# Performance work log

Measured on AMD Instinct MI355X. Metric: run time of the kernel, lower is better.

## Reference

```python
import jax, jax.numpy as jnp
import numpy as np

N_NODES = 50000
N_EDGES = 800000
N_ATOMS = 100
HID = 128
N_LAYERS = 3
OUT_LAYERS = 2
OUT_DIM = 1
N_GRAPHS = 1024
EPS = 1e-12  # F.normalize eps


def setup_inputs() -> dict:
    key = jax.random.key(0)
    ks = jax.random.split(key, 12)
    s = 0.05
    x_ori = jax.random.randint(ks[0], (N_NODES,), 0, N_ATOMS)
    edge_index = jax.random.randint(ks[1], (2, N_EDGES), 0, N_NODES)
    edge_attr = jax.random.normal(ks[2], (N_EDGES, 1), jnp.float32)
    batch_ids = jnp.sort(jax.random.randint(ks[3], (N_NODES,), 0, N_GRAPHS))
    embd_w = jax.random.normal(ks[4], (N_ATOMS, HID), jnp.float32) * s
    gamma_w = jnp.ones((N_LAYERS, N_ATOMS, 1), jnp.float32)  # reset_parameters sets ones
    w_atom_W = jax.random.normal(ks[5], (N_LAYERS, HID, HID), jnp.float32) * s
    w_atom_b = jax.random.normal(ks[6], (N_LAYERS, HID), jnp.float32) * s
    lin_W = jax.random.normal(ks[7], (OUT_LAYERS, HID, HID), jnp.float32) * s
    lin_b = jax.random.normal(ks[8], (OUT_LAYERS, HID), jnp.float32) * s
    wp_W = jax.random.normal(ks[9], (HID, OUT_DIM), jnp.float32) * s
    wp_b = jax.random.normal(ks[10], (OUT_DIM,), jnp.float32) * s
    return dict(x_ori=x_ori, edge_index=edge_index, edge_attr=edge_attr,
                batch_ids=batch_ids, embd_w=embd_w, gamma_w=gamma_w,
                w_atom_W=w_atom_W, w_atom_b=w_atom_b, lin_W=lin_W, lin_b=lin_b,
                wp_W=wp_W, wp_b=wp_b)


def reference(x_ori, edge_index, edge_attr, batch_ids, embd_w, gamma_w,
              w_atom_W, w_atom_b, lin_W, lin_b, wp_W, wp_b):
    src, dst = edge_index[0], edge_index[1]
    x = embd_w[x_ori]  # [N, H]
    for l in range(N_LAYERS):
        h = jax.nn.relu(x @ w_atom_W[l] + w_atom_b[l])            # [N, H]
        gam = jax.nn.sigmoid(gamma_w[l])[x_ori][dst]              # [E, 1]
        ew = jnp.exp(-gam * edge_attr ** 2)                       # [E, 1]
        msg = ew * h[src]                                         # [E, H] gather+weight
        agg = jax.ops.segment_sum(msg, dst, num_segments=N_NODES) # scatter-add
        y = agg + x
        nrm = jnp.maximum(jnp.linalg.norm(y, axis=1, keepdims=True), EPS)
        x = y / nrm                                               # F.normalize(., 2, 1)
    for i in range(OUT_LAYERS):
        x = jax.nn.relu(x @ lin_W[i] + lin_b[i])
    m_x = jax.ops.segment_sum(x, batch_ids, num_segments=N_GRAPHS)  # [G, H]
    props = m_x @ wp_W + wp_b                                      # [G, 1]
    return jnp.squeeze(props, axis=1)                              # [G]
```

## Files before the change

### kernel.cpp

```cpp
#include <hip/hip_runtime.h>
#include <hip/hip_bf16.h>
#include <math.h>

typedef __hip_bfloat16 bf16;
typedef unsigned int uint;
typedef unsigned short ushort;
typedef __attribute__((ext_vector_type(8))) short short8;
typedef __attribute__((ext_vector_type(4))) float f32x4;

#define HID 128
#define NN 50000
#define NE 800000
#define NG 1024
#define NA 100
#define CAP 64

#define NB   98
#define RCAP 10240

__device__ __forceinline__ uint bf16_rne_hi(float f) {
    uint u = __float_as_uint(f);
    return (u + 0x7fffu + ((u >> 16) & 1u)) & 0xffff0000u;
}
__device__ __forceinline__ uint pack_bf16x2(float lo, float hi) {
    return (bf16_rne_hi(lo) >> 16) | bf16_rne_hi(hi);
}
__device__ __forceinline__ ushort bf16_rne(float f) {
    uint u = __float_as_uint(f);
    return (ushort)((u + 0x7fffu + ((u >> 16) & 1u)) >> 16);
}
__device__ __forceinline__ float lof(uint u) { return __uint_as_float(u << 16); }
__device__ __forceinline__ float hif(uint u) { return __uint_as_float(u & 0xffff0000u); }
__device__ __forceinline__ float load_f(const void* p, int i, int f32) {
    return f32 ? ((const float*)p)[i]
               : __uint_as_float((uint)((const ushort*)p)[i] << 16);
}
__device__ __forceinline__ int detect_f32(const void* emb) {
    const ushort* p = (const ushort*)emb;
    int lane = threadIdx.x & 63;
    float v = __uint_as_float((uint)p[lane * 4] << 16);
    int bad0 = (!(v == v) || fabsf(v) > 1e4f || (v != 0.0f && fabsf(v) < 1e-10f));
    float w = __uint_as_float((uint)p[lane * 4 + 2] << 16);
    int bad1 = (!(w == w) || fabsf(w) > 1e4f || (w != 0.0f && fabsf(w) < 1e-10f));
    int cnt = __popcll(__ballot(bad0)) + __popcll(__ballot(bad1));
    return cnt > 16;
}

#define A_BLKS     196
#define EMB_BLKS   ((NN * 64) / 256)
#define PACKW_BLKS (5 * 16384 / 256)
#define CVT_CNT    (300 + 384 + 256 + 128 + 1)
#define CVT_BLKS   5
#define PR_B1      A_BLKS
#define PR_B2      (PR_B1 + EMB_BLKS)
#define PR_B3      (PR_B2 + PACKW_BLKS)
#define PR_B4      (PR_B3 + CVT_BLKS)
#define PR_B5      (PR_B4 + 4)
#define PREP_GRID  (PR_B5 + 1)

__global__ void prep_k(const int* __restrict__ xo, const void* __restrict__ emb,
                       const void* __restrict__ gamw, const void* __restrict__ wAW,
                       const void* __restrict__ wAb, const void* __restrict__ linW,
                       const void* __restrict__ linb, const void* __restrict__ wpW,
                       const void* __restrict__ wpb,
                       const int* __restrict__ esrc, const int* __restrict__ edst,
                       const void* __restrict__ ea,
                       uint* __restrict__ xb, ushort* __restrict__ Wp,
                       float* __restrict__ f_sgam, float* __restrict__ f_wAb,
                       float* __restrict__ f_linb, float* __restrict__ f_wp,
                       float* __restrict__ f_wpb,
                       uint2* __restrict__ rec, int* __restrict__ bcur,
                       float* __restrict__ gpn,
                       float* __restrict__ grf, int* __restrict__ flag) {
    int f32 = detect_f32(emb);
    int b = blockIdx.x, t = threadIdx.x;
    if (b < PR_B1) {
        __shared__ int hist[NB];
        __shared__ int obase[NB];
        if (t < NB) hist[t] = 0;
        __syncthreads();
        int  dv[16];
        uint rv[16];
#pragma unroll
        for (int k = 0; k < 4; ++k) {
            int e = b * 4096 + k * 1024 + t * 4;
            if (e + 3 < NE) {
                int4 s4 = *(const int4*)(esrc + e);
                int4 d4 = *(const int4*)(edst + e);
                float a0, a1, a2, a3;
                if (f32) {
                    float4 f = *(const float4*)((const float*)ea + e);
                    a0 = f.x; a1 = f.y; a2 = f.z; a3 = f.w;
                } else {
                    ushort4 u = *(const ushort4*)((const ushort*)ea + e);
                    a0 = __uint_as_float((uint)u.x << 16);
                    a1 = __uint_as_float((uint)u.y << 16);
                    a2 = __uint_as_float((uint)u.z << 16);
                    a3 = __uint_as_float((uint)u.w << 16);
                }
                atomicAdd(&hist[d4.x >> 9], 1);
                atomicAdd(&hist[d4.y >> 9], 1);
                atomicAdd(&hist[d4.z >> 9], 1);
                atomicAdd(&hist[d4.w >> 9], 1);
                dv[k * 4 + 0] = d4.x; rv[k * 4 + 0] = (uint)(s4.x & 0xffff) | ((uint)bf16_rne(a0 * a0) << 16);
                dv[k * 4 + 1] = d4.y; rv[k * 4 + 1] = (uint)(s4.y & 0xffff) | ((uint)bf16_rne(a1 * a1) << 16);
                dv[k * 4 + 2] = d4.z; rv[k * 4 + 2] = (uint)(s4.z & 0xffff) | ((uint)bf16_rne(a2 * a2) << 16);
                dv[k * 4 + 3] = d4.w; rv[k * 4 + 3] = (uint)(s4.w & 0xffff) | ((uint)bf16_rne(a3 * a3) << 16);
            } else {
                dv[k * 4 + 0] = dv[k * 4 + 1] = dv[k * 4 + 2] = dv[k * 4 + 3] = -1;
                rv[k * 4 + 0] = rv[k * 4 + 1] = rv[k * 4 + 2] = rv[k * 4 + 3] = 0;
            }
        }
        __syncthreads();
        if (t < NB) {
            int c = hist[t];
            obase[t] = c ? atomicAdd(&bcur[t], c) : 0;
            hist[t] = 0;
        }
        __syncthreads();
#pragma unroll
        for (int k = 0; k < 16; ++k) {
            int d = dv[k];
            if (d >= 0) {
                int bb = d >> 9;
                int r = atomicAdd(&hist[bb], 1);
                int idx = obase[bb] + r;
                if (idx < RCAP) rec[bb * RCAP + idx] = make_uint2(rv[k], (uint)d);
            }
        }
    } else if (b < PR_B2) {
        int gidx = (b - PR_B1) * 256 + t;
        int node = gidx >> 6, c2 = gidx & 63;
        int xon = xo[node];
        int base = xon * HID + c2 * 2;
        xb[gidx] = pack_bf16x2(load_f(emb, base, f32), load_f(emb, base + 1, f32));
        if (c2 < 3) {
            float v = load_f(gamw, c2 * 100 + xon, f32);
            gpn[c2 * NN + node] = 1.0f / (1.0f + __expf(-v));
        }
    } else if (b < PR_B3) {
        int t2 = (b - PR_B2) * 256 + t;
        int i   = t2 & 7;
        int n   = (t2 >> 3) & 15;
        int q   = (t2 >> 7) & 3;
        int j16 = (t2 >> 9) & 7;
        int ks  = (t2 >> 12) & 3;
        int mat = t2 >> 14;
        int k = ks * 32 + q * 8 + i;
        int j = j16 * 16 + n;
        const void* W = (mat < 3) ? wAW : linW;
        int off = ((mat < 3) ? mat : (mat - 3)) * 16384 + k * HID + j;
        Wp[t2] = bf16_rne(load_f(W, off, f32));
    } else if (b < PR_B4) {
        int idx = (b - PR_B3) * 256 + t;
        if (idx < 300) {
            float v = load_f(gamw, idx, f32);
            f_sgam[idx] = 1.0f / (1.0f + __expf(-v));
        } else if (idx < 684) {
            f_wAb[idx - 300] = load_f(wAb, idx - 300, f32);
        } else if (idx < 940) {
            f_linb[idx - 684] = load_f(linb, idx - 684, f32);
        } else if (idx < 1068) {
            f_wp[idx - 940] = load_f(wpW, idx - 940, f32);
        } else if (idx < CVT_CNT) {
            f_wpb[0] = load_f(wpb, 0, f32);
        }
    } else if (b < PR_B5) {
        grf[(b - PR_B4) * 256 + t] = 0.0f;
    } else {
        if (t == 0) *flag = f32;
    }
}

__device__ __forceinline__ void gemm_core(const uint* __restrict__ xb,
                                          const ushort* __restrict__ Wp,
                                          const float* __restrict__ bias,
                                          int m0, int lane,
                                          f32x4 acc0[8], f32x4 acc1[8]) {
    int ln15 = lane & 15;
    int q    = lane >> 4;
    int mA = min(m0 + ln15, NN - 1);
    int mB = min(m0 + 16 + ln15, NN - 1);
    const short8* A8 = (const short8*)xb;
    const short8* B8 = (const short8*)Wp;
#pragma unroll
    for (int j16 = 0; j16 < 8; ++j16) {
        float bv = bias[j16 * 16 + ln15];
        acc0[j16] = (f32x4){bv, bv, bv, bv};
        acc1[j16] = acc0[j16];
    }
#pragma unroll
    for (int ks = 0; ks < 4; ++ks) {
        short8 a0 = A8[mA * 16 + ks * 4 + q];
        short8 a1 = A8[mB * 16 + ks * 4 + q];
#pragma unroll
        for (int j16 = 0; j16 < 8; ++j16) {
            short8 b = B8[(ks * 8 + j16) * 64 + q * 16 + ln15];
            acc0[j16] = __builtin_amdgcn_mfma_f32_16x16x32_bf16(a0, b, acc0[j16], 0, 0, 0);
            acc1[j16] = __builtin_amdgcn_mfma_f32_16x16x32_bf16(a1, b, acc1[j16], 0, 0, 0);
        }
    }
}

__device__ __forceinline__ void gemm_store(f32x4 acc0[8], f32x4 acc1[8],
                                           int m0, int lane, uint* __restrict__ outb) {
    int ln15 = lane & 15;
    int q    = lane >> 4;
    ushort* ob = (ushort*)outb;
#pragma unroll
    for (int reg = 0; reg < 4; ++reg) {
        int n0 = m0 + q * 4 + reg;
        int n1 = n0 + 16;
#pragma unroll
        for (int j16 = 0; j16 < 8; ++j16) {
            if (n0 < NN)
                ob[(size_t)n0 * HID + j16 * 16 + ln15] = bf16_rne(fmaxf(acc0[j16][reg], 0.0f));
            if (n1 < NN)
                ob[(size_t)n1 * HID + j16 * 16 + ln15] = bf16_rne(fmaxf(acc1[j16][reg], 0.0f));
        }
    }
}

#define G1_BLKS ((NN + 255) / 256)
__global__ __launch_bounds__(512) void work2_k(const uint* __restrict__ xb,
                                               const ushort* __restrict__ Wp,
                                               const float* __restrict__ bias,
                                               uint* __restrict__ outb,
                                               const uint2* __restrict__ rec,
                                               const int* __restrict__ bcur,
                                               uint* __restrict__ csr,
                                               int* __restrict__ degarr) {
    int b = blockIdx.x, t = threadIdx.x;
    if (b < NB) {
        __shared__ int ldeg[512];
        ldeg[t] = 0;
        __syncthreads();
        int cnt = min(bcur[b], RCAP);
        int nb0 = b << 9;
        for (int i = t; i < cnt; i += 512) {
            uint2 r = rec[b * RCAP + i];
            int dst = (int)r.y;
            int p = atomicAdd(&ldeg[dst - nb0], 1);
            if (p < CAP) csr[dst * CAP + p] = r.x;
        }
        __syncthreads();
        int n = nb0 + t;
        if (n < NN) degarr[n] = min(ldeg[t], CAP);
    } else {
        f32x4 acc0[8], acc1[8];
        int m0 = (b - NB) * 256 + (t >> 6) * 32;
        gemm_core(xb, Wp, bias, m0, t & 63, acc0, acc1);
        gemm_store(acc0, acc1, m0, t & 63, outb);
    }
}

template<int LAST>
__global__ __launch_bounds__(512) void gg_k(const int* __restrict__ degarr,
                                            const uint* __restrict__ csr,
                                            const float* __restrict__ gpn,
                                            const uint* __restrict__ hb_in,
                                            uint* __restrict__ xb,
                                            const ushort* __restrict__ Wp,
                                            const float* __restrict__ bias,
                                            uint* __restrict__ hb_out,
                                            const ushort* __restrict__ Wp2,
                                            const float* __restrict__ bias2,
                                            const float* __restrict__ wp,
                                            const int* __restrict__ batch,
                                            float* __restrict__ grf) {
    __shared__ uint  lds_a[2048];
    __shared__ uint  lds_b[LAST ? 2048 : 1];
    __shared__ float lds_p[LAST ? 256 : 1];
    int t = threadIdx.x;
    int w = t >> 6, lane = t & 63;
    int q = lane >> 4, ln15 = lane & 15;
    int n0 = blockIdx.x * 32;

    int j  = w * 4 + q;
    int n  = n0 + j;
    int nc = min(n, NN - 1);
    int deg = (n < NN) ? degarr[n] : 0;
    const uint* cp = csr + (size_t)nc * CAP;
    float g = gpn[nc];
    float ax0 = 0.f, ax1 = 0.f, ax2 = 0.f, ax3 = 0.f;
    float ay0 = 0.f, ay1 = 0.f, ay2 = 0.f, ay3 = 0.f;
    for (int e = 0; e < deg; e += 4) {
        uint4 c4 = *(const uint4*)(cp + e);
        uint cc[4] = {c4.x, c4.y, c4.z, c4.w};
#pragma unroll
        for (int i = 0; i < 4; ++i) {
            bool vld = (e + i) < deg;
            float wi = vld ? __expf(-g * hif(cc[i])) : 0.0f;
            int   ri = vld ? (int)(cc[i] & 0xffffu) : 0;
            uint4 v  = *(const uint4*)(hb_in + (size_t)ri * 64 + ln15 * 4);
            ax0 = fmaf(wi, lof(v.x), ax0); ay0 = fmaf(wi, hif(v.x), ay0);
            ax1 = fmaf(wi, lof(v.y), ax1); ay1 = fmaf(wi, hif(v.y), ay1);
            ax2 = fmaf(wi, lof(v.z), ax2); ay2 = fmaf(wi, hif(v.z), ay2);
            ax3 = fmaf(wi, lof(v.w), ax3); ay3 = fmaf(wi, hif(v.w), ay3);
        }
    }
    {
        uint4 xv = *(const uint4*)(xb + (size_t)nc * 64 + ln15 * 4);
        float yx0 = ax0 + lof(xv.x), yy0 = ay0 + hif(xv.x);
        float yx1 = ax1 + lof(xv.y), yy1 = ay1 + hif(xv.y);
        float yx2 = ax2 + lof(xv.z), yy2 = ay2 + hif(xv.z);
        float yx3 = ax3 + lof(xv.w), yy3 = ay3 + hif(xv.w);
        float ss = yx0 * yx0 + yy0 * yy0 + yx1 * yx1 + yy1 * yy1
                 + yx2 * yx2 + yy2 * yy2 + yx3 * yx3 + yy3 * yy3;
        ss += __shfl_xor(ss, 1); ss += __shfl_xor(ss, 2);
        ss += __shfl_xor(ss, 4); ss += __shfl_xor(ss, 8);
        float inv = 1.0f / fmaxf(sqrtf(ss), 1e-12f);
        uint4 o;
        o.x = pack_bf16x2(yx0 * inv, yy0 * inv);
        o.y = pack_bf16x2(yx1 * inv, yy1 * inv);
        o.z = pack_bf16x2(yx2 * inv, yy2 * inv);
        o.w = pack_bf16x2(yx3 * inv, yy3 * inv);
        if (!LAST && n < NN) *(uint4*)(xb + (size_t)n * 64 + ln15 * 4) = o;
        int rt = j >> 4, m = j & 15;
        *(uint4*)&lds_a[(((rt * 4 + (ln15 >> 2)) * 64) + (ln15 & 3) * 16 + m) * 4] = o;
    }
    __syncthreads();

    const short8* A8 = (const short8*)lds_a;
    const short8* B8 = (const short8*)Wp;
    f32x4 acc[2];
    {
        float bv = bias[w * 16 + ln15];
        acc[0] = (f32x4){bv, bv, bv, bv};
        acc[1] = acc[0];
    }
#pragma unroll
    for (int ks = 0; ks < 4; ++ks) {
        short8 b = B8[(ks * 8 + w) * 64 + lane];
#pragma unroll
        for (int rt = 0; rt < 2; ++rt) {
            short8 a = A8[(rt * 4 + ks) * 64 + lane];
            acc[rt] = __builtin_amdgcn_mfma_f32_16x16x32_bf16(a, b, acc[rt], 0, 0, 0);
        }
    }
    if (!LAST) {
        ushort* ob = (ushort*)hb_out;
#pragma unroll
        for (int rt = 0; rt < 2; ++rt) {
#pragma unroll
            for (int reg = 0; reg < 4; ++reg) {
                int nn = n0 + rt * 16 + q * 4 + reg;
                if (nn < NN)
                    ob[(size_t)nn * HID + w * 16 + ln15] = bf16_rne(fmaxf(acc[rt][reg], 0.0f));
            }
        }
    } else {
        ushort* sb = (ushort*)lds_b;
        int c  = w * 16 + ln15;
        int c2 = c >> 1, cb = c2 & 3, cq = (c2 >> 2) & 3, cks = c2 >> 4, lohi = c & 1;
#pragma unroll
        for (int rt = 0; rt < 2; ++rt) {
#pragma unroll
            for (int reg = 0; reg < 4; ++reg) {
                int m = q * 4 + reg;
                int uidx = ((rt * 4 + cks) * 64 + cq * 16 + m) * 4 + cb;
                sb[uidx * 2 + lohi] = bf16_rne(fmaxf(acc[rt][reg], 0.0f));
            }
        }
        __syncthreads();
        const short8* A8b = (const short8*)lds_b;
        const short8* B8b = (const short8*)Wp2;
        f32x4 acc3[2];
        {
            float bv = bias2[w * 16 + ln15];
            acc3[0] = (f32x4){bv, bv, bv, bv};
            acc3[1] = acc3[0];
        }
#pragma unroll
        for (int ks = 0; ks < 4; ++ks) {
            short8 bb = B8b[(ks * 8 + w) * 64 + lane];
#pragma unroll
            for (int rt = 0; rt < 2; ++rt) {
                short8 a = A8b[(rt * 4 + ks) * 64 + lane];
                acc3[rt] = __builtin_amdgcn_mfma_f32_16x16x32_bf16(a, bb, acc3[rt], 0, 0, 0);
            }
        }
        float wv = wp[w * 16 + ln15];
#pragma unroll
        for (int rt = 0; rt < 2; ++rt) {
#pragma unroll
            for (int reg = 0; reg < 4; ++reg) {
                float p = fmaxf(acc3[rt][reg], 0.0f) * wv;
                p += __shfl_xor(p, 1); p += __shfl_xor(p, 2);
                p += __shfl_xor(p, 4); p += __shfl_xor(p, 8);
                if (ln15 == 0) lds_p[(rt * 16 + q * 4 + reg) * 8 + w] = p;
            }
        }
        __syncthreads();
        if (t < 32) {
            float s = 0.0f;
#pragma unroll
            for (int k = 0; k < 8; ++k) s += lds_p[t * 8 + k];
            int nn = n0 + t;
            if (nn < NN) atomicAdd(&grf[batch[nn]], s);
        }
    }
}

__global__ void out_k(const float* __restrict__ grf, const float* __restrict__ wpb,
                      void* __restrict__ out, const int* __restrict__ flag) {
    int g = blockIdx.x * 256 + threadIdx.x;
    if (g >= NG) return;
    float r = grf[g] + wpb[0];
    if (*flag) ((float*)out)[g] = r;
    else       ((bf16*)out)[g] = __float2bfloat16(r);
}

extern "C" void kernel_launch(void* const* d_in, const int* in_sizes, int n_in,
                              void* d_out, int out_size, void* d_ws, size_t ws_size,
                              hipStream_t stream) {
    const int*  xo    = (const int*)d_in[0];
    const int*  ei    = (const int*)d_in[1];
    const int*  src   = ei;
    const int*  dst   = ei + NE;
    const void* ea    = d_in[2];
    const int*  batch = (const int*)d_in[3];
    const void* emb   = d_in[4];
    const void* gamw  = d_in[5];
    const void* wAW   = d_in[6];
    const void* wAb   = d_in[7];
    const void* linW  = d_in[8];
    const void* linb  = d_in[9];
    const void* wpW   = d_in[10];
    const void* wpb   = d_in[11];

    uint*  xb     = (uint*)d_ws;
    uint*  hA     = xb + (size_t)NN * 64;
    uint*  hB     = hA + (size_t)NN * 64;
    uint2* rec    = (uint2*)hB;
    uint*  csr    = hB + (size_t)NN * 64;
    int*   degarr = (int*)(csr + (size_t)NN * CAP);
    float* grf    = (float*)(degarr + NN);
    float* P      = grf + NG;
    float* f_sgam = P;
    float* f_wAb  = f_sgam + 304;
    float* f_linb = f_wAb + 384;
    float* f_wp   = f_linb + 256;
    float* f_wpb  = f_wp + 128;
    int*   flag   = (int*)(f_wpb + 8);
    ushort* Wp    = (ushort*)(flag + 8);
    int*   bcur   = (int*)(Wp + 5 * 16384);
    float* gpn    = (float*)(bcur + 128);

    hipMemsetAsync(bcur, 0, NB * sizeof(int), stream);

    prep_k<<<PREP_GRID, 256, 0, stream>>>(xo, emb, gamw, wAW, wAb, linW, linb, wpW, wpb,
                                          src, dst, ea,
                                          xb, Wp, f_sgam, f_wAb, f_linb, f_wp, f_wpb,
                                          rec, bcur, gpn, grf, flag);

    work2_k<<<NB + G1_BLKS, 512, 0, stream>>>(xb, Wp, f_wAb, hA, rec, bcur, csr, degarr);

    const int GG_GRID = (NN + 31) / 32;
    gg_k<0><<<GG_GRID, 512, 0, stream>>>(degarr, csr, gpn,          hA, xb,
                                         Wp + 1 * 16384, f_wAb + 128, hB,
                                         nullptr, nullptr, nullptr, nullptr, nullptr);
    gg_k<0><<<GG_GRID, 512, 0, stream>>>(degarr, csr, gpn + NN,     hB, xb,
                                         Wp + 2 * 16384, f_wAb + 256, hA,
                                         nullptr, nullptr, nullptr, nullptr, nullptr);
    gg_k<1><<<GG_GRID, 512, 0, stream>>>(degarr, csr, gpn + 2 * NN, hA, xb,
                                         Wp + 3 * 16384, f_linb,      nullptr,
                                         Wp + 4 * 16384, f_linb + HID, f_wp, batch, grf);

    out_k<<<(NG + 255) / 256, 256, 0, stream>>>(grf, f_wpb, d_out, flag);
}
```

Baseline: 271.6 us.

## Split fused gather+GEMM into separate gather and GEMM kernels with wave-per-node gather

Replaces the fused gather/normalize/MFMA kernel with a gather kernel that assigns one 64-lane wave per node, splitting its edges across four lane groups with a software-prefetched loop and a shuffle reduction. The per-layer weight GEMM becomes a standalone kernel reusing gemm_core, and only the final layer keeps a fused GEMM+output-MLP+pooling kernel. The goal is more edge-level parallelism and memory latency hiding in the gather than the previous one-quarter-wave-per-node layout gave. In exchange it adds kernel launches and a round trip of x through global memory between gather and GEMM.

```diff
diff --git a/kernel.cpp b/kernel.cpp
--- a/kernel.cpp
+++ b/kernel.cpp
@@ -254,68 +254,90 @@
     }
 }
 
-template<int LAST>
-__global__ __launch_bounds__(512) void gg_k(const int* __restrict__ degarr,
-                                            const uint* __restrict__ csr,
-                                            const float* __restrict__ gpn,
-                                            const uint* __restrict__ hb_in,
-                                            uint* __restrict__ xb,
-                                            const ushort* __restrict__ Wp,
-                                            const float* __restrict__ bias,
-                                            uint* __restrict__ hb_out,
-                                            const ushort* __restrict__ Wp2,
-                                            const float* __restrict__ bias2,
-                                            const float* __restrict__ wp,
-                                            const int* __restrict__ batch,
-                                            float* __restrict__ grf) {
+__global__ __launch_bounds__(256) void gath_k(const int* __restrict__ degarr,
+                                              const uint* __restrict__ csr,
+                                              const float* __restrict__ gpn,
+                                              const uint* __restrict__ hb_in,
+                                              uint* __restrict__ xb) {
+    int t = threadIdx.x;
+    int lane = t & 63;
+    int q = lane >> 4, ln15 = lane & 15;
+    int n = blockIdx.x * 4 + (t >> 6);
+    int deg = degarr[n];
+    const uint* cp = csr + (size_t)n * CAP;
+    float g = gpn[n];
+    float ax0 = 0.f, ax1 = 0.f, ax2 = 0.f, ax3 = 0.f;
+    float ay0 = 0.f, ay1 = 0.f, ay2 = 0.f, ay3 = 0.f;
+    int iters = (deg + 3) >> 2;
+    uint  c_cur = (q < deg) ? cp[q] : 0u;
+    uint4 v_cur = *(const uint4*)(hb_in + (size_t)(c_cur & 0xffffu) * 64 + ln15 * 4);
+    for (int it = 0; it < iters; ++it) {
+        int e_nxt = (it + 1) * 4 + q;
+        uint c_nxt = (e_nxt < deg) ? cp[e_nxt] : 0u;
+        uint4 v_nxt = *(const uint4*)(hb_in + (size_t)(c_nxt & 0xffffu) * 64 + ln15 * 4);
+        float wi = ((it * 4 + q) < deg) ? __expf(-g * hif(c_cur)) : 0.0f;
+        ax0 = fmaf(wi, lof(v_cur.x), ax0); ay0 = fmaf(wi, hif(v_cur.x), ay0);
+        ax1 = fmaf(wi, lof(v_cur.y), ax1); ay1 = fmaf(wi, hif(v_cur.y), ay1);
+        ax2 = fmaf(wi, lof(v_cur.z), ax2); ay2 = fmaf(wi, hif(v_cur.z), ay2);
+        ax3 = fmaf(wi, lof(v_cur.w), ax3); ay3 = fmaf(wi, hif(v_cur.w), ay3);
+        c_cur = c_nxt; v_cur = v_nxt;
+    }
+#pragma unroll
+    for (int m = 16; m <= 32; m <<= 1) {
+        ax0 += __shfl_xor(ax0, m); ay0 += __shfl_xor(ay0, m);
+        ax1 += __shfl_xor(ax1, m); ay1 += __shfl_xor(ay1, m);
+        ax2 += __shfl_xor(ax2, m); ay2 += __shfl_xor(ay2, m);
+        ax3 += __shfl_xor(ax3, m); ay3 += __shfl_xor(ay3, m);
+    }
+    uint4 xv = *(const uint4*)(xb + (size_t)n * 64 + ln15 * 4);
+    float yx0 = ax0 + lof(xv.x), yy0 = ay0 + hif(xv.x);
+    float yx1 = ax1 + lof(xv.y), yy1 = ay1 + hif(xv.y);
+    float yx2 = ax2 + lof(xv.z), yy2 = ay2 + hif(xv.z);
+    float yx3 = ax3 + lof(xv.w), yy3 = ay3 + hif(xv.w);
+    float ss = yx0 * yx0 + yy0 * yy0 + yx1 * yx1 + yy1 * yy1
+             + yx2 * yx2 + yy2 * yy2 + yx3 * yx3 + yy3 * yy3;
+    ss += __shfl_xor(ss, 1); ss += __shfl_xor(ss, 2);
+    ss += __shfl_xor(ss, 4); ss += __shfl_xor(ss, 8);
+    float inv = 1.0f / fmaxf(sqrtf(ss), 1e-12f);
+    uint4 o;
+    o.x = pack_bf16x2(yx0 * inv, yy0 * inv);
+    o.y = pack_bf16x2(yx1 * inv, yy1 * inv);
+    o.z = pack_bf16x2(yx2 * inv, yy2 * inv);
+    o.w = pack_bf16x2(yx3 * inv, yy3 * inv);
+    if (q == 0) *(uint4*)(xb + (size_t)n * 64 + ln15 * 4) = o;
+}
+
+#define GEMM_GRID ((NN + 127) / 128)
+__global__ __launch_bounds__(256) void gemm_k(const uint* __restrict__ xb,
+                                              const ushort* __restrict__ Wp,
+                                              const float* __restrict__ bias,
+                                              uint* __restrict__ outb) {
+    f32x4 acc0[8], acc1[8];
+    int m0 = blockIdx.x * 128 + (threadIdx.x >> 6) * 32;
+    gemm_core(xb, Wp, bias, m0, threadIdx.x & 63, acc0, acc1);
+    gemm_store(acc0, acc1, m0, threadIdx.x & 63, outb);
+}
+
+__global__ __launch_bounds__(512) void ggF_k(const uint* __restrict__ xb,
+                                             const ushort* __restrict__ Wp,
+                                             const float* __restrict__ bias,
+                                             const ushort* __restrict__ Wp2,
+                                             const float* __restrict__ bias2,
+                                             const float* __restrict__ wp,
+                                             const int* __restrict__ batch,
+                                             float* __restrict__ grf) {
     __shared__ uint  lds_a[2048];
-    __shared__ uint  lds_b[LAST ? 2048 : 1];
-    __shared__ float lds_p[LAST ? 256 : 1];
+    __shared__ uint  lds_b[2048];
+    __shared__ float lds_p[256];
     int t = threadIdx.x;
     int w = t >> 6, lane = t & 63;
     int q = lane >> 4, ln15 = lane & 15;
     int n0 = blockIdx.x * 32;
 
-    int j  = w * 4 + q;
-    int n  = n0 + j;
-    int nc = min(n, NN - 1);
-    int deg = (n < NN) ? degarr[n] : 0;
-    const uint* cp = csr + (size_t)nc * CAP;
-    float g = gpn[nc];
-    float ax0 = 0.f, ax1 = 0.f, ax2 = 0.f, ax3 = 0.f;
-    float ay0 = 0.f, ay1 = 0.f, ay2 = 0.f, ay3 = 0.f;
-    for (int e = 0; e < deg; e += 4) {
-        uint4 c4 = *(const uint4*)(cp + e);
-        uint cc[4] = {c4.x, c4.y, c4.z, c4.w};
-#pragma unroll
-        for (int i = 0; i < 4; ++i) {
-            bool vld = (e + i) < deg;
-            float wi = vld ? __expf(-g * hif(cc[i])) : 0.0f;
-            int   ri = vld ? (int)(cc[i] & 0xffffu) : 0;
-            uint4 v  = *(const uint4*)(hb_in + (size_t)ri * 64 + ln15 * 4);
-            ax0 = fmaf(wi, lof(v.x), ax0); ay0 = fmaf(wi, hif(v.x), ay0);
-            ax1 = fmaf(wi, lof(v.y), ax1); ay1 = fmaf(wi, hif(v.y), ay1);
-            ax2 = fmaf(wi, lof(v.z), ax2); ay2 = fmaf(wi, hif(v.z), ay2);
-            ax3 = fmaf(wi, lof(v.w), ax3); ay3 = fmaf(wi, hif(v.w), ay3);
-        }
-    }
     {
-        uint4 xv = *(const uint4*)(xb + (size_t)nc * 64 + ln15 * 4);
-        float yx0 = ax0 + lof(xv.x), yy0 = ay0 + hif(xv.x);
-        float yx1 = ax1 + lof(xv.y), yy1 = ay1 + hif(xv.y);
-        float yx2 = ax2 + lof(xv.z), yy2 = ay2 + hif(xv.z);
-        float yx3 = ax3 + lof(xv.w), yy3 = ay3 + hif(xv.w);
-        float ss = yx0 * yx0 + yy0 * yy0 + yx1 * yx1 + yy1 * yy1
-                 + yx2 * yx2 + yy2 * yy2 + yx3 * yx3 + yy3 * yy3;
-        ss += __shfl_xor(ss, 1); ss += __shfl_xor(ss, 2);
-        ss += __shfl_xor(ss, 4); ss += __shfl_xor(ss, 8);
-        float inv = 1.0f / fmaxf(sqrtf(ss), 1e-12f);
-        uint4 o;
-        o.x = pack_bf16x2(yx0 * inv, yy0 * inv);
-        o.y = pack_bf16x2(yx1 * inv, yy1 * inv);
-        o.z = pack_bf16x2(yx2 * inv, yy2 * inv);
-        o.w = pack_bf16x2(yx3 * inv, yy3 * inv);
-        if (!LAST && n < NN) *(uint4*)(xb + (size_t)n * 64 + ln15 * 4) = o;
+        int j = w * 4 + q;
+        int nc = min(n0 + j, NN - 1);
+        uint4 o = *(const uint4*)(xb + (size_t)nc * 64 + ln15 * 4);
         int rt = j >> 4, m = j & 15;
         *(uint4*)&lds_a[(((rt * 4 + (ln15 >> 2)) * 64) + (ln15 & 3) * 16 + m) * 4] = o;
     }
@@ -338,18 +360,7 @@
             acc[rt] = __builtin_amdgcn_mfma_f32_16x16x32_bf16(a, b, acc[rt], 0, 0, 0);
         }
     }
-    if (!LAST) {
-        ushort* ob = (ushort*)hb_out;
-#pragma unroll
-        for (int rt = 0; rt < 2; ++rt) {
-#pragma unroll
-            for (int reg = 0; reg < 4; ++reg) {
-                int nn = n0 + rt * 16 + q * 4 + reg;
-                if (nn < NN)
-                    ob[(size_t)nn * HID + w * 16 + ln15] = bf16_rne(fmaxf(acc[rt][reg], 0.0f));
-            }
-        }
-    } else {
+    {
         ushort* sb = (ushort*)lds_b;
         int c  = w * 16 + ln15;
         int c2 = c >> 1, cb = c2 & 3, cq = (c2 >> 2) & 3, cks = c2 >> 4, lohi = c & 1;
@@ -362,43 +373,43 @@
                 sb[uidx * 2 + lohi] = bf16_rne(fmaxf(acc[rt][reg], 0.0f));
             }
         }
-        __syncthreads();
-        const short8* A8b = (const short8*)lds_b;
-        const short8* B8b = (const short8*)Wp2;
-        f32x4 acc3[2];
-        {
-            float bv = bias2[w * 16 + ln15];
-            acc3[0] = (f32x4){bv, bv, bv, bv};
-            acc3[1] = acc3[0];
-        }
-#pragma unroll
-        for (int ks = 0; ks < 4; ++ks) {
-            short8 bb = B8b[(ks * 8 + w) * 64 + lane];
-#pragma unroll
-            for (int rt = 0; rt < 2; ++rt) {
-                short8 a = A8b[(rt * 4 + ks) * 64 + lane];
-                acc3[rt] = __builtin_amdgcn_mfma_f32_16x16x32_bf16(a, bb, acc3[rt], 0, 0, 0);
-            }
-        }
-        float wv = wp[w * 16 + ln15];
+    }
+    __syncthreads();
+    const short8* A8b = (const short8*)lds_b;
+    const short8* B8b = (const short8*)Wp2;
+    f32x4 acc3[2];
+    {
+        float bv = bias2[w * 16 + ln15];
+        acc3[0] = (f32x4){bv, bv, bv, bv};
+        acc3[1] = acc3[0];
+    }
+#pragma unroll
+    for (int ks = 0; ks < 4; ++ks) {
+        short8 bb = B8b[(ks * 8 + w) * 64 + lane];
 #pragma unroll
         for (int rt = 0; rt < 2; ++rt) {
-#pragma unroll
-            for (int reg = 0; reg < 4; ++reg) {
-                float p = fmaxf(acc3[rt][reg], 0.0f) * wv;
-                p += __shfl_xor(p, 1); p += __shfl_xor(p, 2);
-                p += __shfl_xor(p, 4); p += __shfl_xor(p, 8);
-                if (ln15 == 0) lds_p[(rt * 16 + q * 4 + reg) * 8 + w] = p;
-            }
-        }
-        __syncthreads();
-        if (t < 32) {
-            float s = 0.0f;
-#pragma unroll
-            for (int k = 0; k < 8; ++k) s += lds_p[t * 8 + k];
-            int nn = n0 + t;
-            if (nn < NN) atomicAdd(&grf[batch[nn]], s);
-        }
+            short8 a = A8b[(rt * 4 + ks) * 64 + lane];
+            acc3[rt] = __builtin_amdgcn_mfma_f32_16x16x32_bf16(a, bb, acc3[rt], 0, 0, 0);
+        }
+    }
+    float wv = wp[w * 16 + ln15];
+#pragma unroll
+    for (int rt = 0; rt < 2; ++rt) {
+#pragma unroll
+        for (int reg = 0; reg < 4; ++reg) {
+            float p = fmaxf(acc3[rt][reg], 0.0f) * wv;
+            p += __shfl_xor(p, 1); p += __shfl_xor(p, 2);
+            p += __shfl_xor(p, 4); p += __shfl_xor(p, 8);
+            if (ln15 == 0) lds_p[(rt * 16 + q * 4 + reg) * 8 + w] = p;
+        }
+    }
+    __syncthreads();
+    if (t < 32) {
+        float s = 0.0f;
+#pragma unroll
+        for (int k = 0; k < 8; ++k) s += lds_p[t * 8 + k];
+        int nn = n0 + t;
+        if (nn < NN) atomicAdd(&grf[batch[nn]], s);
     }
 }
 
@@ -456,16 +467,15 @@
 
     work2_k<<<NB + G1_BLKS, 512, 0, stream>>>(xb, Wp, f_wAb, hA, rec, bcur, csr, degarr);
 
-    const int GG_GRID = (NN + 31) / 32;
-    gg_k<0><<<GG_GRID, 512, 0, stream>>>(degarr, csr, gpn,          hA, xb,
-                                         Wp + 1 * 16384, f_wAb + 128, hB,
-                                         nullptr, nullptr, nullptr, nullptr, nullptr);
-    gg_k<0><<<GG_GRID, 512, 0, stream>>>(degarr, csr, gpn + NN,     hB, xb,
-                                         Wp + 2 * 16384, f_wAb + 256, hA,
-                                         nullptr, nullptr, nullptr, nullptr, nullptr);
-    gg_k<1><<<GG_GRID, 512, 0, stream>>>(degarr, csr, gpn + 2 * NN, hA, xb,
-                                         Wp + 3 * 16384, f_linb,      nullptr,
-                                         Wp + 4 * 16384, f_linb + HID, f_wp, batch, grf);
+    const int GATH_GRID = NN / 4;
+    gath_k<<<GATH_GRID, 256, 0, stream>>>(degarr, csr, gpn,          hA, xb);
+    gemm_k<<<GEMM_GRID, 256, 0, stream>>>(xb, Wp + 1 * 16384, f_wAb + 128, hB);
+    gath_k<<<GATH_GRID, 256, 0, stream>>>(degarr, csr, gpn + NN,     hB, xb);
+    gemm_k<<<GEMM_GRID, 256, 0, stream>>>(xb, Wp + 2 * 16384, f_wAb + 256, hA);
+    gath_k<<<GATH_GRID, 256, 0, stream>>>(degarr, csr, gpn + 2 * NN, hA, xb);
+    ggF_k<<<(NN + 31) / 32, 512, 0, stream>>>(xb, Wp + 3 * 16384, f_linb,
+                                              Wp + 4 * 16384, f_linb + HID,
+                                              f_wp, batch, grf);
 
     out_k<<<(NG + 255) / 256, 256, 0, stream>>>(grf, f_wpb, d_out, flag);
 }
```

Measured after the change: 281.0 us. +3.5%, slower.

## Bin nodes by in-degree so gather blocks process similar-degree nodes

Applied to the files above, without the earlier changes.

Nodes are counted into per-degree bins as the CSR is built, and each gather block then handles a contiguous run of the degree-sorted order instead of consecutive node ids. The aim is to cut wave divergence in the edge loop, where four nodes share a wave and the slowest one sets the loop trip count. In exchange every block runs a serial prefix over 65 bins plus a linear search to map slots to nodes. Row reads, hidden-state writes and the graph pooling now use scattered node addresses, which loses locality for the batch atomics and the output stores.

```diff
diff --git a/kernel.cpp b/kernel.cpp
--- a/kernel.cpp
+++ b/kernel.cpp
@@ -17,6 +17,7 @@
 
 #define NB   98
 #define RCAP 10240
+#define BCAP 16384
 
 __device__ __forceinline__ uint bf16_rne_hi(float f) {
     uint u = __float_as_uint(f);
@@ -229,7 +230,9 @@
                                                const uint2* __restrict__ rec,
                                                const int* __restrict__ bcur,
                                                uint* __restrict__ csr,
-                                               int* __restrict__ degarr) {
+                                               int* __restrict__ degarr,
+                                               int* __restrict__ dcnt,
+                                               uint* __restrict__ binned) {
     int b = blockIdx.x, t = threadIdx.x;
     if (b < NB) {
         __shared__ int ldeg[512];
@@ -245,7 +248,12 @@
         }
         __syncthreads();
         int n = nb0 + t;
-        if (n < NN) degarr[n] = min(ldeg[t], CAP);
+        if (n < NN) {
+            int d = min(ldeg[t], CAP);
+            degarr[n] = d;
+            int slot = atomicAdd(&dcnt[d], 1);
+            if (slot < BCAP) binned[d * BCAP + slot] = (uint)n;
+        }
     } else {
         f32x4 acc0[8], acc1[8];
         int m0 = (b - NB) * 256 + (t >> 6) * 32;
@@ -258,6 +266,8 @@
 __global__ __launch_bounds__(512) void gg_k(const int* __restrict__ degarr,
                                             const uint* __restrict__ csr,
                                             const float* __restrict__ gpn,
+                                            const int* __restrict__ dcnt,
+                                            const uint* __restrict__ binned,
                                             const uint* __restrict__ hb_in,
                                             uint* __restrict__ xb,
                                             const ushort* __restrict__ Wp,
@@ -271,17 +281,38 @@
     __shared__ uint  lds_a[2048];
     __shared__ uint  lds_b[LAST ? 2048 : 1];
     __shared__ float lds_p[LAST ? 256 : 1];
+    __shared__ int   s_off[65], s_cnt[65], s_node[32];
     int t = threadIdx.x;
     int w = t >> 6, lane = t & 63;
     int q = lane >> 4, ln15 = lane & 15;
     int n0 = blockIdx.x * 32;
 
+    if (t < 65) s_cnt[t] = dcnt[t];
+    __syncthreads();
+    if (t == 0) {
+        int run = 0;
+#pragma unroll 1
+        for (int d = 64; d >= 0; --d) { s_off[d] = run; run += s_cnt[d]; }
+    }
+    __syncthreads();
+    if (t < 32) {
+        int s = n0 + t, node = NN - 1;
+        if (s < NN) {
+#pragma unroll 1
+            for (int d = 64; d >= 0; --d) {
+                if (s < s_off[d] + s_cnt[d]) { node = (int)binned[d * BCAP + (s - s_off[d])]; break; }
+            }
+        }
+        s_node[t] = node;
+    }
+    __syncthreads();
+
     int j  = w * 4 + q;
-    int n  = n0 + j;
-    int nc = min(n, NN - 1);
-    int deg = (n < NN) ? degarr[n] : 0;
-    const uint* cp = csr + (size_t)nc * CAP;
-    float g = gpn[nc];
+    int s  = n0 + j;
+    int n  = s_node[j];
+    int deg = (s < NN) ? degarr[n] : 0;
+    const uint* cp = csr + (size_t)n * CAP;
+    float g = gpn[n];
     float ax0 = 0.f, ax1 = 0.f, ax2 = 0.f, ax3 = 0.f;
     float ay0 = 0.f, ay1 = 0.f, ay2 = 0.f, ay3 = 0.f;
     for (int e = 0; e < deg; e += 4) {
@@ -300,7 +331,7 @@
         }
     }
     {
-        uint4 xv = *(const uint4*)(xb + (size_t)nc * 64 + ln15 * 4);
+        uint4 xv = *(const uint4*)(xb + (size_t)n * 64 + ln15 * 4);
         float yx0 = ax0 + lof(xv.x), yy0 = ay0 + hif(xv.x);
         float yx1 = ax1 + lof(xv.y), yy1 = ay1 + hif(xv.y);
         float yx2 = ax2 + lof(xv.z), yy2 = ay2 + hif(xv.z);
@@ -315,7 +346,7 @@
         o.y = pack_bf16x2(yx1 * inv, yy1 * inv);
         o.z = pack_bf16x2(yx2 * inv, yy2 * inv);
         o.w = pack_bf16x2(yx3 * inv, yy3 * inv);
-        if (!LAST && n < NN) *(uint4*)(xb + (size_t)n * 64 + ln15 * 4) = o;
+        if (!LAST && s < NN) *(uint4*)(xb + (size_t)n * 64 + ln15 * 4) = o;
         int rt = j >> 4, m = j & 15;
         *(uint4*)&lds_a[(((rt * 4 + (ln15 >> 2)) * 64) + (ln15 & 3) * 16 + m) * 4] = o;
     }
@@ -344,9 +375,9 @@
         for (int rt = 0; rt < 2; ++rt) {
 #pragma unroll
             for (int reg = 0; reg < 4; ++reg) {
-                int nn = n0 + rt * 16 + q * 4 + reg;
-                if (nn < NN)
-                    ob[(size_t)nn * HID + w * 16 + ln15] = bf16_rne(fmaxf(acc[rt][reg], 0.0f));
+                int r = rt * 16 + q * 4 + reg;
+                if (n0 + r < NN)
+                    ob[(size_t)s_node[r] * HID + w * 16 + ln15] = bf16_rne(fmaxf(acc[rt][reg], 0.0f));
             }
         }
     } else {
@@ -393,11 +424,10 @@
         }
         __syncthreads();
         if (t < 32) {
-            float s = 0.0f;
-#pragma unroll
-            for (int k = 0; k < 8; ++k) s += lds_p[t * 8 + k];
-            int nn = n0 + t;
-            if (nn < NN) atomicAdd(&grf[batch[nn]], s);
+            float sm = 0.0f;
+#pragma unroll
+            for (int k = 0; k < 8; ++k) sm += lds_p[t * 8 + k];
+            if (n0 + t < NN) atomicAdd(&grf[batch[s_node[t]]], sm);
         }
     }
 }
@@ -445,25 +475,28 @@
     int*   flag   = (int*)(f_wpb + 8);
     ushort* Wp    = (ushort*)(flag + 8);
     int*   bcur   = (int*)(Wp + 5 * 16384);
-    float* gpn    = (float*)(bcur + 128);
-
-    hipMemsetAsync(bcur, 0, NB * sizeof(int), stream);
+    int*   dcnt   = bcur + 128;
+    float* gpn    = (float*)(dcnt + 128);
+    uint*  binned = (uint*)(gpn + 3 * NN);
+
+    hipMemsetAsync(bcur, 0, 256 * sizeof(int), stream);
 
     prep_k<<<PREP_GRID, 256, 0, stream>>>(xo, emb, gamw, wAW, wAb, linW, linb, wpW, wpb,
                                           src, dst, ea,
                                           xb, Wp, f_sgam, f_wAb, f_linb, f_wp, f_wpb,
                                           rec, bcur, gpn, grf, flag);
 
-    work2_k<<<NB + G1_BLKS, 512, 0, stream>>>(xb, Wp, f_wAb, hA, rec, bcur, csr, degarr);
+    work2_k<<<NB + G1_BLKS, 512, 0, stream>>>(xb, Wp, f_wAb, hA, rec, bcur, csr, degarr,
+                                              dcnt, binned);
 
     const int GG_GRID = (NN + 31) / 32;
-    gg_k<0><<<GG_GRID, 512, 0, stream>>>(degarr, csr, gpn,          hA, xb,
+    gg_k<0><<<GG_GRID, 512, 0, stream>>>(degarr, csr, gpn,          dcnt, binned, hA, xb,
                                          Wp + 1 * 16384, f_wAb + 128, hB,
                                          nullptr, nullptr, nullptr, nullptr, nullptr);
-    gg_k<0><<<GG_GRID, 512, 0, stream>>>(degarr, csr, gpn + NN,     hB, xb,
+    gg_k<0><<<GG_GRID, 512, 0, stream>>>(degarr, csr, gpn + NN,     dcnt, binned, hB, xb,
                                          Wp + 2 * 16384, f_wAb + 256, hA,
                                          nullptr, nullptr, nullptr, nullptr, nullptr);
-    gg_k<1><<<GG_GRID, 512, 0, stream>>>(degarr, csr, gpn + 2 * NN, hA, xb,
+    gg_k<1><<<GG_GRID, 512, 0, stream>>>(degarr, csr, gpn + 2 * NN, dcnt, binned, hA, xb,
                                          Wp + 3 * 16384, f_linb,      nullptr,
                                          Wp + 4 * 16384, f_linb + HID, f_wp, batch, grf);
 
```

New measurement: 366.5 us. 1.35x slower.
